# Optimization experiments

Measured on AMD Instinct MI355X. Metric: run time of the kernel, lower is better.

Reference implementation:

```python
import jax, jax.numpy as jnp
import numpy as np

NUM_SITES = 64
BOND_DIM = 64
PHYS_DIM = 2
BATCH = 8192
INIT_STD = 0.125  # 1/sqrt(bond_dim)
EPS_AMP = 1e-12
EPS_LOG = 1e-30


def setup_inputs() -> dict:
    key = jax.random.key(0)
    k_cfg, k_l, k_b, k_r = jax.random.split(key, 4)
    configurations = jax.random.randint(k_cfg, (BATCH, NUM_SITES), 0, PHYS_DIM, dtype=jnp.int32)
    left = jax.random.normal(k_l, (PHYS_DIM, BOND_DIM), dtype=jnp.float32) * INIT_STD
    bulk = jax.random.normal(k_b, (NUM_SITES - 2, BOND_DIM, PHYS_DIM, BOND_DIM), dtype=jnp.float32) * INIT_STD
    right = jax.random.normal(k_r, (BOND_DIM, PHYS_DIM), dtype=jnp.float32) * INIT_STD
    return {"configurations": configurations, "left": left, "bulk": bulk, "right": right}


def _psi(configurations, left, bulk, right):
    # configurations: [B, S] int; left: [d, D]; bulk: [S-2, D, d, D]; right: [D, d]
    B = configurations.shape[0]
    env0 = left[configurations[:, 0]]  # [B, D]
    cfg_mid = configurations[:, 1:-1].T  # [S-2, B]

    def step(env, xs):
        site_t, idx = xs  # site_t: [D, d, D], idx: [B]
        D = site_t.shape[0]
        # env @ site (contract left bond), then gather the per-sample physical slice
        tmp = (env @ site_t.reshape(D, -1)).reshape(B, PHYS_DIM, D)  # [B, d, D]
        env = jnp.take_along_axis(tmp, idx[:, None, None], axis=1)[:, 0, :]  # [B, D]
        return env, None

    env, _ = jax.lax.scan(step, env0, (bulk, cfg_mid))
    cols = jnp.take(right, configurations[:, -1], axis=1).T  # [B, D]
    return jnp.sum(env * cols, axis=1)  # [B]


def _log_norm(left, bulk, right):
    env0 = left.T @ left  # [D, D]  (real dtype -> conj trivial)

    def step(carry, site_t):
        env, log_scale = carry
        sm = jnp.transpose(site_t, (1, 0, 2))  # [d, D, D]
        env = jnp.einsum('pdi,de,pej->ij', sm, env, sm)  # sum_p A_p^H env A_p
        scale = jnp.maximum(jnp.max(jnp.abs(env)), EPS_LOG)
        return (env / scale, log_scale + jnp.log(scale)), None

    (env, log_scale), _ = jax.lax.scan(step, (env0, jnp.zeros((), left.dtype)), bulk)
    z = jnp.sum(right * (env @ right))
    return jnp.log(jnp.maximum(z, EPS_LOG)) + log_scale


def reference(configurations, left, bulk, right):
    psi = _psi(configurations, left, bulk, right)
    abs_sq = jnp.maximum(psi * psi, EPS_AMP)
    log_z = _log_norm(left, bulk, right)
    nll = -(jnp.log(abs_sq) - log_z)
    return jnp.mean(nll)
```

## Files before the change

kernel.cpp:

```cpp
#include <hip/hip_runtime.h>
#include <math.h>

#define NBULK 62

typedef __attribute__((ext_vector_type(8))) short bf8_t;
typedef __attribute__((ext_vector_type(4))) float f4_t;

#define MFMA16(a, b, c) __builtin_amdgcn_mfma_f32_16x16x32_bf16((a), (b), (c), 0, 0, 0)

__device__ __forceinline__ unsigned short f2bf(float f) {
    unsigned int u = __float_as_uint(f);
    return (unsigned short)((u + 0x7FFFu + ((u >> 16) & 1u)) >> 16);
}
__device__ __forceinline__ float bf2f(unsigned short h) {
    return __uint_as_float(((unsigned int)h) << 16);
}
__device__ __forceinline__ unsigned cvtpk(float lo, float hi) {
    unsigned r;
    asm("v_cvt_pk_bf16_f32 %0, %1, %2" : "=v"(r) : "v"(lo), "v"(hi));
    return r;
}

__device__ __forceinline__ void gload16(const void* g, void* l) {
    __builtin_amdgcn_global_load_lds(
        (const __attribute__((address_space(1))) unsigned int*)g,
        (__attribute__((address_space(3))) unsigned int*)l, 16, 0, 0);
}

#define WS_E_OFF   1024
#define WS_B_OFF   6144
#define WS_NFF_OFF 45056
#define WS_NFB_OFF 1060864


extern "C" __global__ __launch_bounds__(256)
void mps_precompute(const float* __restrict__ bulkG,
                    unsigned short* __restrict__ NFfG,
                    unsigned short* __restrict__ NFbG,
                    float* __restrict__ wsF)
{
    __shared__ unsigned short Ff[8192];
    __shared__ unsigned short Fb[8192];
    const int s = blockIdx.x, tid = threadIdx.x;
    if (s == 0 && tid == 0) {
        wsF[0] = 0.f; wsF[1] = 0.f; wsF[2] = 0.f; wsF[3] = 0.f;
    }
    const float4* src = (const float4*)(bulkG + (size_t)s * 8192);
    for (int c = 0; c < 8; ++c) {
        int idx = tid + c * 256;
        float4 v = src[idx];
        int f  = idx * 4;
        int kk = f >> 7;
        int p  = (f >> 6) & 1;
        int j0 = f & 63;
        float vals[4] = {v.x, v.y, v.z, v.w};
        int qf = (kk >> 2) & 3, rf = kk & 3, mf = kk >> 4;
        int ksf = mf >> 1, jjf = (mf & 1) * 4 + rf;
        int tb = kk >> 4, lnb = kk & 15;
        #pragma unroll
        for (int t2 = 0; t2 < 4; ++t2) {
            int j = j0 + t2;
            unsigned short b = f2bf(vals[t2]);
            int tf = j >> 4, lnf = j & 15;
            Ff[((p * 4 + tf) * 2 + ksf) * 512 + (qf * 16 + lnf) * 8 + jjf] = b;
            int qb = (j >> 2) & 3, rb = j & 3, mb = j >> 4;
            int ksb = mb >> 1, jjb = (mb & 1) * 4 + rb;
            Fb[((p * 4 + tb) * 2 + ksb) * 512 + (qb * 16 + lnb) * 8 + jjb] = b;
        }
    }
    __syncthreads();
    const uint4* ff4 = (const uint4*)Ff;
    const uint4* fb4 = (const uint4*)Fb;
    uint4* fg = (uint4*)(NFfG + (size_t)s * 8192);
    uint4* bg = (uint4*)(NFbG + (size_t)s * 8192);
    for (int c = 0; c < 4; ++c) {
        int idx = tid + c * 256;
        fg[idx] = ff4[idx];
        bg[idx] = fb4[idx];
    }
}

__device__ __forceinline__ void pfetch(uint4 (&F)[16], const char* tb, int l16)
{
    #pragma unroll
    for (int i = 0; i < 16; ++i)
        F[i] = *(const uint4*)(tb + i * 1024 + l16);
}

__device__ __forceinline__ void pstep(f4_t (&a)[2][4], const uint4 (&F)[16],
                                      const bf8_t (&B)[2])
{
    #pragma unroll
    for (int p = 0; p < 2; ++p)
        #pragma unroll
        for (int mt = 0; mt < 4; ++mt) { f4_t z = {0.f, 0.f, 0.f, 0.f}; a[p][mt] = z; }
    #pragma unroll
    for (int ks = 0; ks < 2; ++ks)
        #pragma unroll
        for (int p = 0; p < 2; ++p)
            #pragma unroll
            for (int mt = 0; mt < 4; ++mt)
                a[p][mt] = MFMA16(*(const bf8_t*)&F[(p * 4 + mt) * 2 + ks], B[ks], a[p][mt]);
}

__device__ __forceinline__ void ppack(bf8_t (&B)[2], const f4_t (&a)[2][4], bool takeB)
{
    #pragma unroll
    for (int ks = 0; ks < 2; ++ks) {
        unsigned w[4];
        #pragma unroll
        for (int d = 0; d < 4; ++d) {
            int mt = 2 * ks + (d >> 1), r = (d & 1) * 2;
            float x0 = takeB ? a[1][mt][r]     : a[0][mt][r];
            float x1 = takeB ? a[1][mt][r + 1] : a[0][mt][r + 1];
            w[d] = cvtpk(x0, x1);
        }
        uint4 u = {w[0], w[1], w[2], w[3]};
        B[ks] = *(const bf8_t*)&u;
    }
}

extern "C" __global__ __launch_bounds__(256, 1)
void mps_main(const int* __restrict__ cfgG, const float* __restrict__ leftG,
              const float* __restrict__ rightG, float* __restrict__ wsF,
              const unsigned short* __restrict__ NFfG,
              const unsigned short* __restrict__ NFbG)
{
    extern __shared__ char smem[];
    const int tid  = threadIdx.x;
    const int bid  = blockIdx.x;
    const int wv   = tid >> 6;
    const int lane = tid & 63;
    const int ln   = lane & 15, q = lane >> 4;
    const int l16  = lane * 16;

    if (bid >= 2) {
        const char* NF = (const char*)NFfG;
        uint4 Fa[16], Fb[16];
        pfetch(Fa, NF, l16);
        pfetch(Fb, NF + 16384, l16);
        const int s0 = (bid - 2) * 64 + wv * 16;
        unsigned part = 0;
        {
            const int4* crow = (const int4*)(cfgG + (size_t)(s0 + ln) * 64 + q * 16);
            #pragma unroll
            for (int c = 0; c < 4; ++c) {
                int4 v = crow[c];
                part |= (unsigned)(v.x & 1) << (c * 4 + 0);
                part |= (unsigned)(v.y & 1) << (c * 4 + 1);
                part |= (unsigned)(v.z & 1) << (c * 4 + 2);
                part |= (unsigned)(v.w & 1) << (c * 4 + 3);
            }
        }
        unsigned pp   = __shfl_xor(part, 16);
        unsigned comb = (q & 1) ? (pp | (part << 16)) : (part | (pp << 16));
        unsigned selLo = __shfl(comb, ln);
        unsigned selHi = __shfl(comb, ln + 32);

        bf8_t B[2];
        {
            const float* lp = leftG + (selLo & 1u) * 64;
            #pragma unroll
            for (int ks = 0; ks < 2; ++ks) {
                unsigned w[4];
                #pragma unroll
                for (int d = 0; d < 4; ++d) {
                    int k0 = 16 * (2 * ks + (d >> 1)) + 4 * q + 2 * (d & 1);
                    w[d] = (unsigned)f2bf(lp[k0]) | ((unsigned)f2bf(lp[k0 + 1]) << 16);
                }
                uint4 u = {w[0], w[1], w[2], w[3]};
                B[ks] = *(const bf8_t*)&u;
            }
        }
        f4_t a[2][4];
        #define SELBIT(i) ((bool)((((i) < 32) ? (selLo >> (i)) : (selHi >> ((i) - 32))) & 1u))
        for (int t = 0; t < 60; t += 2) {
            pstep(a, Fa, B);
            pfetch(Fa, NF + (size_t)(t + 2) * 16384, l16);
            __builtin_amdgcn_sched_barrier(0);
            ppack(B, a, SELBIT(t + 1));
            pstep(a, Fb, B);
            pfetch(Fb, NF + (size_t)(t + 3) * 16384, l16);
            __builtin_amdgcn_sched_barrier(0);
            ppack(B, a, SELBIT(t + 2));
        }
        pstep(a, Fa, B);
        ppack(B, a, SELBIT(61));
        pstep(a, Fb, B);
        {
            bool tb2 = SELBIT(62);
            int selL = (int)(selHi >> 31) & 1;
            float psum = 0.f;
            #pragma unroll
            for (int mt = 0; mt < 4; ++mt)
                #pragma unroll
                for (int r = 0; r < 4; ++r) {
                    float v = tb2 ? a[1][mt][r] : a[0][mt][r];
                    psum = fmaf(v, rightG[(16 * mt + 4 * q + r) * 2 + selL], psum);
                }
            psum += __shfl_xor(psum, 16);
            psum += __shfl_xor(psum, 32);
            float lp2 = (lane < 16) ? logf(fmaxf(psum * psum, 1e-12f)) : 0.f;
            #pragma unroll
            for (int o = 1; o < 64; o <<= 1) lp2 += __shfl_xor(lp2, o);
            if (lane == 0) atomicAdd(&wsF[0], lp2);
        }
        #undef SELBIT
    } else {
        unsigned short* Ms0 = (unsigned short*)smem;
        unsigned short* Ms1 = Ms0 + 8192;
        unsigned short* XsS = Ms1 + 8192;
        float* wredS = (float*)(XsS + 8192);

        const bool fwd = (bid == 0);
        const char* NF = fwd ? (const char*)NFfG : (const char*)NFbG;
        {
            int st = fwd ? 0 : 61;
            const char* g = NF + (size_t)st * 16384;
            for (int c = 0; c < 4; ++c) {
                int chunk = wv * 4 + c;
                gload16(g + chunk * 1024 + (size_t)lane * 16, (char*)Ms0 + chunk * 1024);
            }
        }
        bf8_t A1[4][2];
        {
            float li0[4], li1[4];
            #pragma unroll
            for (int mt = 0; mt < 4; ++mt) {
                int m = mt * 16 + ln;
                li0[mt] = fwd ? leftG[m]      : rightG[m * 2];
                li1[mt] = fwd ? leftG[64 + m] : rightG[m * 2 + 1];
            }
            #pragma unroll
            for (int ks = 0; ks < 2; ++ks) {
                float k0v[8], k1v[8];
                #pragma unroll
                for (int jj = 0; jj < 8; ++jj) {
                    int K = 16 * (2 * ks + (jj >> 2)) + 4 * q + (jj & 3);
                    k0v[jj] = fwd ? leftG[K]      : rightG[K * 2];
                    k1v[jj] = fwd ? leftG[64 + K] : rightG[K * 2 + 1];
                }
                #pragma unroll
                for (int mt = 0; mt < 4; ++mt) {
                    unsigned w[4];
                    #pragma unroll
                    for (int d = 0; d < 4; ++d) {
                        float x0 = li0[mt] * k0v[2 * d]     + li1[mt] * k1v[2 * d];
                        float x1 = li0[mt] * k0v[2 * d + 1] + li1[mt] * k1v[2 * d + 1];
                        w[d] = cvtpk(x0, x1);
                    }
                    uint4 u = {w[0], w[1], w[2], w[3]};
                    A1[mt][ks] = *(const bf8_t*)&u;
                }
            }
        }
        float lsum = 0.f;
        f4_t acc2[4];
        for (int k = 0; k < 31; ++k) {
            __syncthreads();
            if (k > 0) {
                #pragma unroll
                for (int mt = 0; mt < 4; ++mt)
                    #pragma unroll
                    for (int ks = 0; ks < 2; ++ks)
                        A1[mt][ks] = *(const bf8_t*)&XsS[((k & 1) * 8 + mt * 2 + ks) * 512
                                                         + lane * 8];
            }
            const unsigned short* Msrc = (k & 1) ? Ms1 : Ms0;
            uint4 F[16];
            #pragma unroll
            for (int i = 0; i < 16; ++i)
                F[i] = *(const uint4*)(Msrc + i * 512 + lane * 8);
            bf8_t B1f[2][2];
            #pragma unroll
            for (int p = 0; p < 2; ++p)
                #pragma unroll
                for (int ks = 0; ks < 2; ++ks)
                    B1f[p][ks] = *(const bf8_t*)(Msrc + ((p * 4 + wv) * 2 + ks) * 512
                                                 + lane * 8);
            if (k + 1 < 31) {
                int sn = fwd ? (k + 1) : (61 - (k + 1));
                const char* g = NF + (size_t)sn * 16384;
                char* l = (char*)((k & 1) ? Ms0 : Ms1);
                for (int c = 0; c < 4; ++c) {
                    int chunk = wv * 4 + c;
                    gload16(g + chunk * 1024 + (size_t)lane * 16, l + chunk * 1024);
                }
            }
            float inv = 1.f;
            if (k > 0) {
                const float* wp = wredS + ((k - 1) & 1) * 4;
                float mm = fmaxf(fmaxf(wp[0], wp[1]), fmaxf(wp[2], wp[3]));
                float sc = fmaxf(mm, 1e-30f);
                inv = 1.f / sc;
                lsum += logf(sc);
            }
            #pragma unroll
            for (int mt = 0; mt < 4; ++mt) { f4_t z = {0.f, 0.f, 0.f, 0.f}; acc2[mt] = z; }
            #pragma unroll
            for (int p = 0; p < 2; ++p) {
                f4_t acc1[4];
                #pragma unroll
                for (int mt = 0; mt < 4; ++mt) { f4_t z = {0.f, 0.f, 0.f, 0.f}; acc1[mt] = z; }
                #pragma unroll
                for (int ks = 0; ks < 2; ++ks)
                    #pragma unroll
                    for (int mt = 0; mt < 4; ++mt)
                        acc1[mt] = MFMA16(A1[mt][ks], B1f[p][ks], acc1[mt]);
                bf8_t B2[2];
                #pragma unroll
                for (int ks = 0; ks < 2; ++ks) {
                    unsigned w[4];
                    #pragma unroll
                    for (int d = 0; d < 4; ++d) {
                        int mt = 2 * ks + (d >> 1), r = (d & 1) * 2;
                        w[d] = cvtpk(acc1[mt][r], acc1[mt][r + 1]);
                    }
                    uint4 u = {w[0], w[1], w[2], w[3]};
                    B2[ks] = *(const bf8_t*)&u;
                }
                #pragma unroll
                for (int ks = 0; ks < 2; ++ks)
                    #pragma unroll
                    for (int mt = 0; mt < 4; ++mt)
                        acc2[mt] = MFMA16(*(const bf8_t*)&F[(p * 4 + mt) * 2 + ks], B2[ks],
                                          acc2[mt]);
            }
            float mx = 0.f;
            #pragma unroll
            for (int mt = 0; mt < 4; ++mt)
                #pragma unroll
                for (int r = 0; r < 4; ++r) {
                    float x = acc2[mt][r] * inv;
                    acc2[mt][r] = x;
                    mx = fmaxf(mx, fabsf(x));
                }
            #pragma unroll
            for (int ks = 0; ks < 2; ++ks) {
                unsigned w[4];
                #pragma unroll
                for (int d = 0; d < 4; ++d) {
                    int mt = 2 * ks + (d >> 1), r = (d & 1) * 2;
                    w[d] = cvtpk(acc2[mt][r], acc2[mt][r + 1]);
                }
                uint4 u = {w[0], w[1], w[2], w[3]};
                *(uint4*)&XsS[(((k + 1) & 1) * 8 + wv * 2 + ks) * 512 + lane * 8] = u;
            }
            #pragma unroll
            for (int o = 32; o > 0; o >>= 1) mx = fmaxf(mx, __shfl_xor(mx, o));
            if (lane == 0) wredS[(k & 1) * 4 + wv] = mx;
        }
        float* dst = wsF + (fwd ? WS_E_OFF : WS_B_OFF);
        #pragma unroll
        for (int mt = 0; mt < 4; ++mt)
            #pragma unroll
            for (int r = 0; r < 4; ++r)
                dst[(16 * mt + 4 * q + r) * 64 + wv * 16 + ln] = acc2[mt][r];
        if (tid == 0) wsF[fwd ? 1 : 2] = lsum;
    }
}

extern "C" __global__ void mps_finalize(const float* __restrict__ wsF, float* __restrict__ out)
{
    const int lane = threadIdx.x;
    const float* E  = wsF + WS_E_OFF;
    const float* Bm = wsF + WS_B_OFF;
    float a = 0.f;
    #pragma unroll 8
    for (int j = 0; j < 64; ++j)
        a = fmaf(E[j * 64 + lane], Bm[j * 64 + lane], a);
    #pragma unroll
    for (int off = 32; off > 0; off >>= 1)
        a += __shfl_down(a, off);
    if (lane == 0) {
        const float z = fmaxf(a, 1e-30f);
        const float log_z = logf(z) + wsF[1] + wsF[2];
        out[0] = log_z - wsF[0] * (1.0f / 8192.0f);
    }
}

extern "C" void kernel_launch(void* const* d_in, const int* in_sizes, int n_in,
                              void* d_out, int out_size, void* d_ws, size_t ws_size,
                              hipStream_t stream)
{
    const int*   cfg   = (const int*)d_in[0];
    const float* left  = (const float*)d_in[1];
    const float* bulk  = (const float*)d_in[2];
    const float* right = (const float*)d_in[3];
    float* wsF = (float*)d_ws;
    unsigned short* NFf = (unsigned short*)((char*)d_ws + WS_NFF_OFF);
    unsigned short* NFb = (unsigned short*)((char*)d_ws + WS_NFB_OFF);

    mps_precompute<<<dim3(62), dim3(256), 0, stream>>>(bulk, NFf, NFb, wsF);
    mps_main<<<dim3(130), dim3(256), 49216, stream>>>(cfg, left, right, wsF, NFf, NFb);
    mps_finalize<<<dim3(1), dim3(64), 0, stream>>>(wsF, (float*)d_out);
}
```

Before: 104.7 us.

## Fuse finalize into main kernel and split accumulator chains in serial loop

Removes the separate finalize kernel by having the last-finishing block (detected via an atomic counter in workspace) compute the final log-norm and loss. In the serial norm-contraction loop, the next-site async prefetch is issued before LDS reads, and the second MFMA stage accumulates into two independent chains summed afterwards to shorten dependency latency. Relies on the counter word being zeroed before each launch and adds a fence and atomic per block.

Result: slower. 181.2 us (+73.1%).

```diff
diff --git a/kernel.cpp b/kernel.cpp
--- a/kernel.cpp
+++ b/kernel.cpp
@@ -124,9 +124,11 @@
 void mps_main(const int* __restrict__ cfgG, const float* __restrict__ leftG,
               const float* __restrict__ rightG, float* __restrict__ wsF,
               const unsigned short* __restrict__ NFfG,
-              const unsigned short* __restrict__ NFbG)
+              const unsigned short* __restrict__ NFbG,
+              float* __restrict__ outG)
 {
     extern __shared__ char smem[];
+    __shared__ int lastf;
     const int tid  = threadIdx.x;
     const int bid  = blockIdx.x;
     const int wv   = tid >> 6;
@@ -215,8 +217,7 @@
         const bool fwd = (bid == 0);
         const char* NF = fwd ? (const char*)NFfG : (const char*)NFbG;
         {
-            int st = fwd ? 0 : 61;
-            const char* g = NF + (size_t)st * 16384;
+            const char* g = NF + (size_t)(fwd ? 0 : 61) * 16384;
             for (int c = 0; c < 4; ++c) {
                 int chunk = wv * 4 + c;
                 gload16(g + chunk * 1024 + (size_t)lane * 16, (char*)Ms0 + chunk * 1024);
@@ -255,29 +256,9 @@
             }
         }
         float lsum = 0.f;
-        f4_t acc2[4];
+        f4_t acc2s[2][4];
         for (int k = 0; k < 31; ++k) {
             __syncthreads();
-            if (k > 0) {
-                #pragma unroll
-                for (int mt = 0; mt < 4; ++mt)
-                    #pragma unroll
-                    for (int ks = 0; ks < 2; ++ks)
-                        A1[mt][ks] = *(const bf8_t*)&XsS[((k & 1) * 8 + mt * 2 + ks) * 512
-                                                         + lane * 8];
-            }
-            const unsigned short* Msrc = (k & 1) ? Ms1 : Ms0;
-            uint4 F[16];
-            #pragma unroll
-            for (int i = 0; i < 16; ++i)
-                F[i] = *(const uint4*)(Msrc + i * 512 + lane * 8);
-            bf8_t B1f[2][2];
-            #pragma unroll
-            for (int p = 0; p < 2; ++p)
-                #pragma unroll
-                for (int ks = 0; ks < 2; ++ks)
-                    B1f[p][ks] = *(const bf8_t*)(Msrc + ((p * 4 + wv) * 2 + ks) * 512
-                                                 + lane * 8);
             if (k + 1 < 31) {
                 int sn = fwd ? (k + 1) : (61 - (k + 1));
                 const char* g = NF + (size_t)sn * 16384;
@@ -287,6 +268,26 @@
                     gload16(g + chunk * 1024 + (size_t)lane * 16, l + chunk * 1024);
                 }
             }
+            if (k > 0) {
+                #pragma unroll
+                for (int mt = 0; mt < 4; ++mt)
+                    #pragma unroll
+                    for (int ks = 0; ks < 2; ++ks)
+                        A1[mt][ks] = *(const bf8_t*)&XsS[((k & 1) * 8 + mt * 2 + ks) * 512
+                                                         + lane * 8];
+            }
+            const unsigned short* Msrc = (k & 1) ? Ms1 : Ms0;
+            uint4 F[16];
+            #pragma unroll
+            for (int i = 0; i < 16; ++i)
+                F[i] = *(const uint4*)(Msrc + i * 512 + lane * 8);
+            bf8_t B1f[2][2];
+            #pragma unroll
+            for (int p = 0; p < 2; ++p)
+                #pragma unroll
+                for (int ks = 0; ks < 2; ++ks)
+                    B1f[p][ks] = *(const bf8_t*)(Msrc + ((p * 4 + wv) * 2 + ks) * 512
+                                                 + lane * 8);
             float inv = 1.f;
             if (k > 0) {
                 const float* wp = wredS + ((k - 1) & 1) * 4;
@@ -296,7 +297,12 @@
                 lsum += logf(sc);
             }
             #pragma unroll
-            for (int mt = 0; mt < 4; ++mt) { f4_t z = {0.f, 0.f, 0.f, 0.f}; acc2[mt] = z; }
+            for (int p = 0; p < 2; ++p)
+                #pragma unroll
+                for (int mt = 0; mt < 4; ++mt) {
+                    f4_t z = {0.f, 0.f, 0.f, 0.f};
+                    acc2s[p][mt] = z;
+                }
             #pragma unroll
             for (int p = 0; p < 2; ++p) {
                 f4_t acc1[4];
@@ -323,16 +329,16 @@
                 for (int ks = 0; ks < 2; ++ks)
                     #pragma unroll
                     for (int mt = 0; mt < 4; ++mt)
-                        acc2[mt] = MFMA16(*(const bf8_t*)&F[(p * 4 + mt) * 2 + ks], B2[ks],
-                                          acc2[mt]);
+                        acc2s[p][mt] = MFMA16(*(const bf8_t*)&F[(p * 4 + mt) * 2 + ks],
+                                              B2[ks], acc2s[p][mt]);
             }
             float mx = 0.f;
             #pragma unroll
             for (int mt = 0; mt < 4; ++mt)
                 #pragma unroll
                 for (int r = 0; r < 4; ++r) {
-                    float x = acc2[mt][r] * inv;
-                    acc2[mt][r] = x;
+                    float x = (acc2s[0][mt][r] + acc2s[1][mt][r]) * inv;
+                    acc2s[0][mt][r] = x;
                     mx = fmaxf(mx, fabsf(x));
                 }
             #pragma unroll
@@ -341,7 +347,7 @@
                 #pragma unroll
                 for (int d = 0; d < 4; ++d) {
                     int mt = 2 * ks + (d >> 1), r = (d & 1) * 2;
-                    w[d] = cvtpk(acc2[mt][r], acc2[mt][r + 1]);
+                    w[d] = cvtpk(acc2s[0][mt][r], acc2s[0][mt][r + 1]);
                 }
                 uint4 u = {w[0], w[1], w[2], w[3]};
                 *(uint4*)&XsS[(((k + 1) & 1) * 8 + wv * 2 + ks) * 512 + lane * 8] = u;
@@ -355,27 +361,32 @@
         for (int mt = 0; mt < 4; ++mt)
             #pragma unroll
             for (int r = 0; r < 4; ++r)
-                dst[(16 * mt + 4 * q + r) * 64 + wv * 16 + ln] = acc2[mt][r];
+                dst[(16 * mt + 4 * q + r) * 64 + wv * 16 + ln] = acc2s[0][mt][r];
         if (tid == 0) wsF[fwd ? 1 : 2] = lsum;
     }
-}
-
-extern "C" __global__ void mps_finalize(const float* __restrict__ wsF, float* __restrict__ out)
-{
-    const int lane = threadIdx.x;
-    const float* E  = wsF + WS_E_OFF;
-    const float* Bm = wsF + WS_B_OFF;
-    float a = 0.f;
-    #pragma unroll 8
-    for (int j = 0; j < 64; ++j)
-        a = fmaf(E[j * 64 + lane], Bm[j * 64 + lane], a);
-    #pragma unroll
-    for (int off = 32; off > 0; off >>= 1)
-        a += __shfl_down(a, off);
-    if (lane == 0) {
-        const float z = fmaxf(a, 1e-30f);
-        const float log_z = logf(z) + wsF[1] + wsF[2];
-        out[0] = log_z - wsF[0] * (1.0f / 8192.0f);
+
+    __threadfence();
+    if (tid == 0)
+        lastf = (atomicAdd((int*)&wsF[3], 1) == (int)gridDim.x - 1);
+    __syncthreads();
+    if (lastf) {
+        __threadfence();
+        if (wv == 0) {
+            const float* E  = wsF + WS_E_OFF;
+            const float* Bm = wsF + WS_B_OFF;
+            float a2 = 0.f;
+            #pragma unroll 8
+            for (int c2 = 0; c2 < 64; ++c2)
+                a2 = fmaf(E[c2 * 64 + lane], Bm[c2 * 64 + lane], a2);
+            #pragma unroll
+            for (int o = 32; o > 0; o >>= 1)
+                a2 += __shfl_down(a2, o);
+            if (lane == 0) {
+                const float z = fmaxf(a2, 1e-30f);
+                const float log_z = logf(z) + wsF[1] + wsF[2];
+                outG[0] = log_z - wsF[0] * (1.0f / 8192.0f);
+            }
+        }
     }
 }
 
@@ -392,6 +403,6 @@
     unsigned short* NFb = (unsigned short*)((char*)d_ws + WS_NFB_OFF);
 
     mps_precompute<<<dim3(62), dim3(256), 0, stream>>>(bulk, NFf, NFb, wsF);
-    mps_main<<<dim3(130), dim3(256), 49216, stream>>>(cfg, left, right, wsF, NFf, NFb);
-    mps_finalize<<<dim3(1), dim3(64), 0, stream>>>(wsF, (float*)d_out);
-}
+    mps_main<<<dim3(130), dim3(256), 49216, stream>>>(cfg, left, right, wsF, NFf, NFb,
+                                                      (float*)d_out);
+}
```
